# Kernel optimization log

Measured on AMD Instinct MI355X. Metric: run time of the kernel, lower is better.

Reference implementation:

```python
import jax, jax.numpy as jnp
import numpy as np
from jax import lax

H = 2048   # n_hidden
D = 1024   # vect_dim
T = 4096   # timesteps per sequence


def _gru_seq(x, W_ih, W_hh, b_ih, b_hh):
    """Run a GRUCell (PyTorch gate math, gate order r,z,n) over x: [T, D] -> final h [H]."""
    # Precompute all input-to-hidden projections in one batched GEMM: [T, 3H]
    xp = x @ W_ih.T + b_ih

    def step(h, xt):
        hp = h @ W_hh.T + b_hh               # [3H]
        xr, xz, xn = jnp.split(xt, 3)
        hr, hz, hn = jnp.split(hp, 3)
        r = jax.nn.sigmoid(xr + hr)
        z = jax.nn.sigmoid(xz + hz)
        n = jnp.tanh(xn + r * hn)
        h_new = (1.0 - z) * n + z * h
        return h_new, None

    h0 = jnp.zeros((H,), dtype=x.dtype)
    h_final, _ = lax.scan(step, h0, xp)
    return h_final


def setup_inputs() -> dict:
    key = jax.random.key(0)
    ks = jax.random.split(key, 16)
    s_g = 1.0 / np.sqrt(H)   # torch GRUCell init scale
    s_f1 = 1.0 / np.sqrt(2 * H)
    s_f2 = 1.0 / np.sqrt(256)
    return {
        "x1": jax.random.normal(ks[0], (T, D), dtype=jnp.float32),
        "x2": jax.random.normal(ks[1], (T, D), dtype=jnp.float32),
        "W_ih1": jax.random.uniform(ks[2], (3 * H, D), jnp.float32, -s_g, s_g),
        "W_hh1": jax.random.uniform(ks[3], (3 * H, H), jnp.float32, -s_g, s_g),
        "b_ih1": jax.random.uniform(ks[4], (3 * H,), jnp.float32, -s_g, s_g),
        "b_hh1": jax.random.uniform(ks[5], (3 * H,), jnp.float32, -s_g, s_g),
        "W_ih2": jax.random.uniform(ks[6], (3 * H, D), jnp.float32, -s_g, s_g),
        "W_hh2": jax.random.uniform(ks[7], (3 * H, H), jnp.float32, -s_g, s_g),
        "b_ih2": jax.random.uniform(ks[8], (3 * H,), jnp.float32, -s_g, s_g),
        "b_hh2": jax.random.uniform(ks[9], (3 * H,), jnp.float32, -s_g, s_g),
        "fc1_w": jax.random.uniform(ks[10], (256, 2 * H), jnp.float32, -s_f1, s_f1),
        "fc1_b": jax.random.uniform(ks[11], (256,), jnp.float32, -s_f1, s_f1),
        "fc2_w": jax.random.uniform(ks[12], (3, 256), jnp.float32, -s_f2, s_f2),
        "fc2_b": jax.random.uniform(ks[13], (3,), jnp.float32, -s_f2, s_f2),
    }


def reference(x1, x2, W_ih1, W_hh1, b_ih1, b_hh1, W_ih2, W_hh2, b_ih2, b_hh2,
              fc1_w, fc1_b, fc2_w, fc2_b):
    h1 = _gru_seq(x1, W_ih1, W_hh1, b_ih1, b_hh1)   # [H]
    h2 = _gru_seq(x2, W_ih2, W_hh2, b_ih2, b_hh2)   # [H]
    out = jnp.concatenate([h1, h2])[None, :]         # [1, 2H]
    out = jax.nn.relu(out @ fc1_w.T + fc1_b)         # [1, 256]
    out = out @ fc2_w.T + fc2_b                      # [1, 3]
    return jax.nn.log_softmax(out, axis=1)
```

## Files before the change

### kernel.cpp

```cpp
#include <hip/hip_runtime.h>
#include <hip/hip_bf16.h>

constexpr int kH  = 2048;
constexpr int kD  = 1024;
constexpr int kT  = 4096;
constexpr int kTH = 3 * kH;
constexpr int kNB = 256;


__global__ void init_sync_kernel(unsigned* __restrict__ sync) {
    sync[blockIdx.x * 1024 + threadIdx.x] = 0u;
}

__global__ __launch_bounds__(256) void gemm_xp_kernel(
    const float* __restrict__ x1, const float* __restrict__ x2,
    const float* __restrict__ Wih1, const float* __restrict__ Wih2,
    const float* __restrict__ bih1, const float* __restrict__ bih2,
    float* __restrict__ xp1, float* __restrict__ xp2) {
    const float* x  = blockIdx.z ? x2   : x1;
    const float* W  = blockIdx.z ? Wih2 : Wih1;
    const float* bi = blockIdx.z ? bih2 : bih1;
    float*       xp = blockIdx.z ? xp2  : xp1;

    __shared__ float As[16][68];
    __shared__ float Bs[16][68];

    const int tid  = threadIdx.x;
    const int tx   = tid & 15, ty = tid >> 4;
    const int lrow = tid >> 2;
    const int lk   = (tid & 3) * 4;
    const int m0   = blockIdx.y * 64;
    const int n0   = blockIdx.x * 64;

    float acc[4][4] = {};

    for (int k0 = 0; k0 < kD; k0 += 16) {
        float4 av = *(const float4*)(x + (size_t)(m0 + lrow) * kD + k0 + lk);
        float4 bv = *(const float4*)(W + (size_t)(n0 + lrow) * kD + k0 + lk);
        __syncthreads();
        As[lk + 0][lrow] = av.x; As[lk + 1][lrow] = av.y;
        As[lk + 2][lrow] = av.z; As[lk + 3][lrow] = av.w;
        Bs[lk + 0][lrow] = bv.x; Bs[lk + 1][lrow] = bv.y;
        Bs[lk + 2][lrow] = bv.z; Bs[lk + 3][lrow] = bv.w;
        __syncthreads();
#pragma unroll
        for (int kk = 0; kk < 16; ++kk) {
            float4 a = *(const float4*)&As[kk][ty * 4];
            float4 b = *(const float4*)&Bs[kk][tx * 4];
            float aa[4] = {a.x, a.y, a.z, a.w};
            float bb[4] = {b.x, b.y, b.z, b.w};
#pragma unroll
            for (int i = 0; i < 4; ++i)
#pragma unroll
                for (int j = 0; j < 4; ++j)
                    acc[i][j] = fmaf(aa[i], bb[j], acc[i][j]);
        }
    }

    float4 bb4 = *(const float4*)(bi + n0 + tx * 4);
    float bArr[4] = {bb4.x, bb4.y, bb4.z, bb4.w};
#pragma unroll
    for (int i = 0; i < 4; ++i) {
        float4 o;
        o.x = acc[i][0] + bArr[0];
        o.y = acc[i][1] + bArr[1];
        o.z = acc[i][2] + bArr[2];
        o.w = acc[i][3] + bArr[3];
        *(float4*)(xp + (size_t)(m0 + ty * 4 + i) * kTH + n0 + tx * 4) = o;
    }
}

__global__ __launch_bounds__(512, 2) void gru_pair_kernel(
    const float* __restrict__ xp1, const float* __restrict__ xp2,
    const float* __restrict__ Whh1, const float* __restrict__ Whh2,
    const float* __restrict__ bhh1, const float* __restrict__ bhh2,
    float* __restrict__ h1b0, float* __restrict__ h1b1,
    float* __restrict__ h2b0, float* __restrict__ h2b1,
    unsigned* __restrict__ sync) {
    const int tid  = threadIdx.x;
    const int lane = tid & 63;
    const int wv   = tid >> 6;
    const int b    = blockIdx.x;
    const int s    = b >> 7;
    const int lb   = b & 127;
    const int i0   = lb * 16;
    const float* xp  = s ? xp2  : xp1;
    const float* Whh = s ? Whh2 : Whh1;
    const float* bhh = s ? bhh2 : bhh1;
    float* hb0 = s ? h2b0 : h1b0;
    float* hb1 = s ? h2b1 : h1b1;
    unsigned* flags = sync + s * 2048;

    __shared__ float h_s[kH];
    __shared__ float hp_s[48];
    __shared__ float xp_s[2][48];

    float w[6][32];
    float bias[6];
#pragma unroll
    for (int p = 0; p < 6; ++p) {
        const int lr = wv * 6 + p;
        const int g  = lr >> 4, j = lr & 15;
        const int rg = g * kH + i0 + j;
        bias[p] = bhh[rg];
        const float* wr = Whh + (size_t)rg * kH;
#pragma unroll
        for (int e = 0; e < 8; ++e) {
            float4 v = *(const float4*)(wr + e * 256 + lane * 4);
            w[p][e * 4 + 0] = v.x; w[p][e * 4 + 1] = v.y;
            w[p][e * 4 + 2] = v.z; w[p][e * 4 + 3] = v.w;
        }
    }
    {
        const int k = tid * 4;
        *(float4*)&h_s[k] = make_float4(0.f, 0.f, 0.f, 0.f);
    }
    if (tid < 48) {
        xp_s[0][tid] = xp[(size_t)(tid >> 4) * kH + i0 + (tid & 15)];
    }
    __syncthreads();

    for (int t = 0; t < kT; ++t) {
        float acc[6];
#pragma unroll
        for (int p = 0; p < 6; ++p) acc[p] = 0.f;
#pragma unroll
        for (int e = 0; e < 8; ++e) {
            const float4 hv = *(const float4*)&h_s[e * 256 + lane * 4];
#pragma unroll
            for (int p = 0; p < 6; ++p) {
                acc[p] = fmaf(w[p][e * 4 + 0], hv.x, acc[p]);
                acc[p] = fmaf(w[p][e * 4 + 1], hv.y, acc[p]);
                acc[p] = fmaf(w[p][e * 4 + 2], hv.z, acc[p]);
                acc[p] = fmaf(w[p][e * 4 + 3], hv.w, acc[p]);
            }
        }
#pragma unroll
        for (int p = 0; p < 6; ++p) {
            float a = acc[p];
#pragma unroll
            for (int off = 32; off; off >>= 1) a += __shfl_down(a, off, 64);
            if (lane == 0) hp_s[wv * 6 + p] = a + bias[p];
        }
        __syncthreads();

        float* dst = ((t + 1) & 1) ? hb1 : hb0;
        if (wv == 0) {
            if (lane < 16) {
                const int i = i0 + lane;
                const float xr = xp_s[t & 1][lane];
                const float xz = xp_s[t & 1][16 + lane];
                const float xn = xp_s[t & 1][32 + lane];
                const float r = 1.f / (1.f + expf(-(xr + hp_s[lane])));
                const float z = 1.f / (1.f + expf(-(xz + hp_s[16 + lane])));
                const float n = tanhf(xn + r * hp_s[32 + lane]);
                const float hn = (1.f - z) * n + z * h_s[i];
                __hip_atomic_store(&dst[i], hn, __ATOMIC_RELAXED,
                                   __HIP_MEMORY_SCOPE_AGENT);
            }
            asm volatile("s_waitcnt vmcnt(0)" ::: "memory");
            if (lane == 0) {
                __hip_atomic_store(&flags[lb * 16], (unsigned)(t + 1),
                                   __ATOMIC_RELAXED, __HIP_MEMORY_SCOPE_AGENT);
            }
        } else if (wv == 1) {
            if (t + 1 < kT && lane < 48) {
                xp_s[(t + 1) & 1][lane] =
                    xp[(size_t)(t + 1) * kTH + (size_t)(lane >> 4) * kH + i0 +
                       (lane & 15)];
            }
            const unsigned tgt = (unsigned)(t + 1);
            const unsigned* fa = flags + lane * 16;
            const unsigned* fb = flags + (lane + 64) * 16;
            for (;;) {
                unsigned f1 = __hip_atomic_load(fa, __ATOMIC_RELAXED,
                                                __HIP_MEMORY_SCOPE_AGENT);
                unsigned f2 = __hip_atomic_load(fb, __ATOMIC_RELAXED,
                                                __HIP_MEMORY_SCOPE_AGENT);
                if (__all((f1 >= tgt) && (f2 >= tgt))) break;
                __builtin_amdgcn_s_sleep(1);
            }
        }
        __syncthreads();

        {
            const int k = tid * 4;
            unsigned long long lo = __hip_atomic_load(
                (const unsigned long long*)&dst[k], __ATOMIC_RELAXED,
                __HIP_MEMORY_SCOPE_AGENT);
            unsigned long long hi = __hip_atomic_load(
                (const unsigned long long*)&dst[k + 2], __ATOMIC_RELAXED,
                __HIP_MEMORY_SCOPE_AGENT);
            float4 hv;
            hv.x = __uint_as_float((unsigned)(lo & 0xffffffffu));
            hv.y = __uint_as_float((unsigned)(lo >> 32));
            hv.z = __uint_as_float((unsigned)(hi & 0xffffffffu));
            hv.w = __uint_as_float((unsigned)(hi >> 32));
            *(float4*)&h_s[k] = hv;
        }
        __syncthreads();
    }
}

__global__ __launch_bounds__(256) void head_kernel(
    const float* __restrict__ h1, const float* __restrict__ h2,
    const float* __restrict__ fc1w, const float* __restrict__ fc1b,
    const float* __restrict__ fc2w, const float* __restrict__ fc2b,
    float* __restrict__ out) {
    __shared__ float cat[2 * kH];
    __shared__ float o1[256];
    __shared__ float logits[3];
    const int tid  = threadIdx.x;
    const int lane = tid & 63;
    const int wave = tid >> 6;

    for (int k = tid; k < kH; k += 256) {
        cat[k]      = h1[k];
        cat[kH + k] = h2[k];
    }
    __syncthreads();

    for (int r = wave; r < 256; r += 4) {
        const float* wr = fc1w + (size_t)r * (2 * kH);
        float acc = 0.f;
        for (int j = lane; j < 2 * kH; j += 64) acc = fmaf(wr[j], cat[j], acc);
#pragma unroll
        for (int off = 32; off; off >>= 1) acc += __shfl_down(acc, off, 64);
        if (lane == 0) o1[r] = fmaxf(acc + fc1b[r], 0.f);
    }
    __syncthreads();

    if (tid < 3) {
        float acc = fc2b[tid];
        const float* wr = fc2w + tid * 256;
        for (int j = 0; j < 256; ++j) acc = fmaf(wr[j], o1[j], acc);
        logits[tid] = acc;
    }
    __syncthreads();

    if (tid == 0) {
        float m = fmaxf(logits[0], fmaxf(logits[1], logits[2]));
        float s = expf(logits[0] - m) + expf(logits[1] - m) + expf(logits[2] - m);
        float ls = logf(s);
        out[0] = logits[0] - m - ls;
        out[1] = logits[1] - m - ls;
        out[2] = logits[2] - m - ls;
    }
}

extern "C" void kernel_launch(void* const* d_in, const int* in_sizes, int n_in,
                              void* d_out, int out_size, void* d_ws,
                              size_t ws_size, hipStream_t stream) {
    const float* x1   = (const float*)d_in[0];
    const float* x2   = (const float*)d_in[1];
    const float* Wih1 = (const float*)d_in[2];
    const float* Whh1 = (const float*)d_in[3];
    const float* bih1 = (const float*)d_in[4];
    const float* bhh1 = (const float*)d_in[5];
    const float* Wih2 = (const float*)d_in[6];
    const float* Whh2 = (const float*)d_in[7];
    const float* bih2 = (const float*)d_in[8];
    const float* bhh2 = (const float*)d_in[9];
    const float* fc1w = (const float*)d_in[10];
    const float* fc1b = (const float*)d_in[11];
    const float* fc2w = (const float*)d_in[12];
    const float* fc2b = (const float*)d_in[13];
    float* out = (float*)d_out;

    char* ws = (char*)d_ws;
    float* xp1 = (float*)ws;
    float* xp2 = xp1 + (size_t)kT * kTH;
    float* hb  = xp2 + (size_t)kT * kTH;
    float* h1b0 = hb;
    float* h1b1 = hb + kH;
    float* h2b0 = hb + 2 * kH;
    float* h2b1 = hb + 3 * kH;
    unsigned* sync = (unsigned*)(hb + 4 * kH);

    init_sync_kernel<<<4, 1024, 0, stream>>>(sync);

    gemm_xp_kernel<<<dim3(kTH / 64, kT / 64, 2), 256, 0, stream>>>(
        x1, x2, Wih1, Wih2, bih1, bih2, xp1, xp2);

    gru_pair_kernel<<<dim3(kNB), dim3(512), 0, stream>>>(
        xp1, xp2, Whh1, Whh2, bhh1, bhh2, h1b0, h1b1, h2b0, h2b1, sync);

    head_kernel<<<1, 256, 0, stream>>>(h1b0, h2b0, fc1w, fc1b, fc2w, fc2b, out);
}
```

Before: 20.89 ms.

## Pack step tag with hidden value to replace separate flag barrier

Each hidden value is now published as a 64-bit word holding the step index and the float, so consumers poll the data directly instead of waiting on per-block flags and then re-reading the hidden buffer. This drops the vmcnt wait, the flag store, one __syncthreads, and the separate data load after the flag poll. The last step writes to a dedicated final buffer for the head kernel. Every thread now spins on four 64-bit loads, which raises polling traffic on the published buffer, and launch bounds change to one block per CU.

```diff
diff --git a/kernel.cpp b/kernel.cpp
--- a/kernel.cpp
+++ b/kernel.cpp
@@ -8,8 +8,8 @@
 constexpr int kNB = 256;
 
 
-__global__ void init_sync_kernel(unsigned* __restrict__ sync) {
-    sync[blockIdx.x * 1024 + threadIdx.x] = 0u;
+__global__ void init_pub_kernel(unsigned long long* __restrict__ pub) {
+    pub[blockIdx.x * 1024 + threadIdx.x] = 0ull;
 }
 
 __global__ __launch_bounds__(256) void gemm_xp_kernel(
@@ -70,13 +70,12 @@
     }
 }
 
-__global__ __launch_bounds__(512, 2) void gru_pair_kernel(
+__global__ __launch_bounds__(512, 1) void gru_pair_kernel(
     const float* __restrict__ xp1, const float* __restrict__ xp2,
     const float* __restrict__ Whh1, const float* __restrict__ Whh2,
     const float* __restrict__ bhh1, const float* __restrict__ bhh2,
-    float* __restrict__ h1b0, float* __restrict__ h1b1,
-    float* __restrict__ h2b0, float* __restrict__ h2b1,
-    unsigned* __restrict__ sync) {
+    unsigned long long* __restrict__ pub,
+    float* __restrict__ hfinal) {
     const int tid  = threadIdx.x;
     const int lane = tid & 63;
     const int wv   = tid >> 6;
@@ -87,9 +86,7 @@
     const float* xp  = s ? xp2  : xp1;
     const float* Whh = s ? Whh2 : Whh1;
     const float* bhh = s ? bhh2 : bhh1;
-    float* hb0 = s ? h2b0 : h1b0;
-    float* hb1 = s ? h2b1 : h1b1;
-    unsigned* flags = sync + s * 2048;
+    unsigned long long* pubs = pub + (size_t)s * 2 * kH;
 
     __shared__ float h_s[kH];
     __shared__ float hp_s[48];
@@ -144,7 +141,7 @@
         }
         __syncthreads();
 
-        float* dst = ((t + 1) & 1) ? hb1 : hb0;
+        unsigned long long* dst = pubs + (size_t)((t + 1) & 1) * kH;
         if (wv == 0) {
             if (lane < 16) {
                 const int i = i0 + lane;
@@ -155,13 +152,15 @@
                 const float z = 1.f / (1.f + expf(-(xz + hp_s[16 + lane])));
                 const float n = tanhf(xn + r * hp_s[32 + lane]);
                 const float hn = (1.f - z) * n + z * h_s[i];
-                __hip_atomic_store(&dst[i], hn, __ATOMIC_RELAXED,
-                                   __HIP_MEMORY_SCOPE_AGENT);
-            }
-            asm volatile("s_waitcnt vmcnt(0)" ::: "memory");
-            if (lane == 0) {
-                __hip_atomic_store(&flags[lb * 16], (unsigned)(t + 1),
-                                   __ATOMIC_RELAXED, __HIP_MEMORY_SCOPE_AGENT);
+                if (t == kT - 1) {
+                    hfinal[s * kH + i] = hn;
+                } else {
+                    const unsigned long long pk =
+                        ((unsigned long long)(unsigned)(t + 1) << 32) |
+                        (unsigned long long)__float_as_uint(hn);
+                    __hip_atomic_store(&dst[i], pk, __ATOMIC_RELAXED,
+                                       __HIP_MEMORY_SCOPE_AGENT);
+                }
             }
         } else if (wv == 1) {
             if (t + 1 < kT && lane < 48) {
@@ -169,34 +168,35 @@
                     xp[(size_t)(t + 1) * kTH + (size_t)(lane >> 4) * kH + i0 +
                        (lane & 15)];
             }
+        }
+        if (t + 1 == kT) break;
+
+        {
             const unsigned tgt = (unsigned)(t + 1);
-            const unsigned* fa = flags + lane * 16;
-            const unsigned* fb = flags + (lane + 64) * 16;
+            const int base = tid * 4;
+            unsigned long long v0, v1, v2, v3;
             for (;;) {
-                unsigned f1 = __hip_atomic_load(fa, __ATOMIC_RELAXED,
-                                                __HIP_MEMORY_SCOPE_AGENT);
-                unsigned f2 = __hip_atomic_load(fb, __ATOMIC_RELAXED,
-                                                __HIP_MEMORY_SCOPE_AGENT);
-                if (__all((f1 >= tgt) && (f2 >= tgt))) break;
+                v0 = __hip_atomic_load(&dst[base + 0], __ATOMIC_RELAXED,
+                                       __HIP_MEMORY_SCOPE_AGENT);
+                v1 = __hip_atomic_load(&dst[base + 1], __ATOMIC_RELAXED,
+                                       __HIP_MEMORY_SCOPE_AGENT);
+                v2 = __hip_atomic_load(&dst[base + 2], __ATOMIC_RELAXED,
+                                       __HIP_MEMORY_SCOPE_AGENT);
+                v3 = __hip_atomic_load(&dst[base + 3], __ATOMIC_RELAXED,
+                                       __HIP_MEMORY_SCOPE_AGENT);
+                if (((unsigned)(v0 >> 32) == tgt) &
+                    ((unsigned)(v1 >> 32) == tgt) &
+                    ((unsigned)(v2 >> 32) == tgt) &
+                    ((unsigned)(v3 >> 32) == tgt))
+                    break;
                 __builtin_amdgcn_s_sleep(1);
             }
-        }
-        __syncthreads();
-
-        {
-            const int k = tid * 4;
-            unsigned long long lo = __hip_atomic_load(
-                (const unsigned long long*)&dst[k], __ATOMIC_RELAXED,
-                __HIP_MEMORY_SCOPE_AGENT);
-            unsigned long long hi = __hip_atomic_load(
-                (const unsigned long long*)&dst[k + 2], __ATOMIC_RELAXED,
-                __HIP_MEMORY_SCOPE_AGENT);
             float4 hv;
-            hv.x = __uint_as_float((unsigned)(lo & 0xffffffffu));
-            hv.y = __uint_as_float((unsigned)(lo >> 32));
-            hv.z = __uint_as_float((unsigned)(hi & 0xffffffffu));
-            hv.w = __uint_as_float((unsigned)(hi >> 32));
-            *(float4*)&h_s[k] = hv;
+            hv.x = __uint_as_float((unsigned)v0);
+            hv.y = __uint_as_float((unsigned)v1);
+            hv.z = __uint_as_float((unsigned)v2);
+            hv.w = __uint_as_float((unsigned)v3);
+            *(float4*)&h_s[base] = hv;
         }
         __syncthreads();
     }
@@ -270,20 +270,17 @@
     char* ws = (char*)d_ws;
     float* xp1 = (float*)ws;
     float* xp2 = xp1 + (size_t)kT * kTH;
-    float* hb  = xp2 + (size_t)kT * kTH;
-    float* h1b0 = hb;
-    float* h1b1 = hb + kH;
-    float* h2b0 = hb + 2 * kH;
-    float* h2b1 = hb + 3 * kH;
-    unsigned* sync = (unsigned*)(hb + 4 * kH);
-
-    init_sync_kernel<<<4, 1024, 0, stream>>>(sync);
+    unsigned long long* pub = (unsigned long long*)(xp2 + (size_t)kT * kTH);
+    float* hfinal = (float*)(pub + 4 * kH);
+
+    init_pub_kernel<<<8, 1024, 0, stream>>>(pub);
 
     gemm_xp_kernel<<<dim3(kTH / 64, kT / 64, 2), 256, 0, stream>>>(
         x1, x2, Wih1, Wih2, bih1, bih2, xp1, xp2);
 
     gru_pair_kernel<<<dim3(kNB), dim3(512), 0, stream>>>(
-        xp1, xp2, Whh1, Whh2, bhh1, bhh2, h1b0, h1b1, h2b0, h2b1, sync);
-
-    head_kernel<<<1, 256, 0, stream>>>(h1b0, h2b0, fc1w, fc1b, fc2w, fc2b, out);
-}
+        xp1, xp2, Whh1, Whh2, bhh1, bhh2, pub, hfinal);
+
+    head_kernel<<<1, 256, 0, stream>>>(hfinal, hfinal + kH, fc1w, fc1b, fc2w,
+                                       fc2b, out);
+}
```

Result: slower. 22.10 ms (+5.8%).
